# Kernel tuning notes

Measured on AMD Instinct MI355X. Metric: run time of the kernel, lower is better.

Reference implementation:

```python
import jax, jax.numpy as jnp
import numpy as np

E, D, H, K, N = 8, 512, 2048, 2, 1024  # experts, d_model, d_hidden, top_k, tokens
EPS = 1e-5


def _moe_linear(x, idx, W, b):
    # x: (M, in); idx: (M,) expert id per row; W: (E, out, in); b: (E, out)
    # Brute-force: compute per-expert dense GEMMs, select via one-hot (matches
    # BruteForceMoELinear math: y[i] = x[i] @ W[idx[i]].T + b[idx[i]]).
    m = jax.nn.one_hot(idx, W.shape[0], dtype=x.dtype)  # (M, E)
    y = jnp.einsum('me,eoi,mi->mo', m, W, x)
    return y + jnp.take(b, idx, axis=0)


def _forward(inp, gate_w, gate_b, w1, b1, w2, b2, ln_w, ln_b):
    # NaiveGate: linear -> top_k -> softmax over top-k logits
    logits = inp @ gate_w.T + gate_b              # (N, E)
    top_val, top_idx = jax.lax.top_k(logits, K)   # (N, K)
    score = jax.nn.softmax(top_val, axis=-1)      # (N, K)
    # repeat_interleave tokens, dispatch to experts
    x = jnp.repeat(inp, K, axis=0)                # (N*K, D)
    idx = top_idx.reshape(-1)                     # (N*K,)
    x = _moe_linear(x, idx, w1, b1)               # (N*K, H)
    x = jax.nn.gelu(x, approximate=False)         # torch F.gelu default = erf
    x = _moe_linear(x, idx, w2, b2)               # (N*K, D)
    x = x.reshape(N, K, D)
    x = jnp.einsum('nk,nkd->nd', score, x)        # bmm((N,1,K),(N,K,D)) combine
    # post layer norm (pre_lnorm=False)
    mu = jnp.mean(x, axis=-1, keepdims=True)
    var = jnp.var(x, axis=-1, keepdims=True)
    return (x - mu) * jax.lax.rsqrt(var + EPS) * ln_w + ln_b


def setup_inputs() -> dict:
    key = jax.random.key(0)
    ks = jax.random.split(key, 8)
    s = 0.02
    return {
        'inp': jax.random.normal(ks[0], (N, D), dtype=jnp.float32),
        'gate_w': s * jax.random.normal(ks[1], (E, D), dtype=jnp.float32),
        'gate_b': jnp.zeros((E,), dtype=jnp.float32),
        'w1': s * jax.random.normal(ks[2], (E, H, D), dtype=jnp.float32),
        'b1': jnp.zeros((E, H), dtype=jnp.float32),
        'w2': s * jax.random.normal(ks[3], (E, D, H), dtype=jnp.float32),
        'b2': jnp.zeros((E, D), dtype=jnp.float32),
        'ln_w': jnp.ones((D,), dtype=jnp.float32),
        'ln_b': jnp.zeros((D,), dtype=jnp.float32),
    }


def reference(inp, gate_w, gate_b, w1, b1, w2, b2, ln_w, ln_b):
    return _forward(inp, gate_w, gate_b, w1, b1, w2, b2, ln_w, ln_b)
```

## Files before the change

kernel.cpp:

```cpp
#include <hip/hip_runtime.h>
#include <cstdint>
#include <cstddef>

typedef _Float16 half_t;
typedef _Float16 half8 __attribute__((ext_vector_type(8)));
typedef float floatx4 __attribute__((ext_vector_type(4)));

#define E_ 8
#define D_ 512
#define H_ 2048
#define NTOK 1024
#define NP 2048
#define TM 128
#define MAX_TILES 24

__device__ __forceinline__ float gelu_f(float x) {
    return 0.5f * x * (1.0f + erff(x * 0.7071067811865476f));
}

__device__ __forceinline__ void gload_lds16(const half_t* g, half_t* l) {
    __builtin_amdgcn_global_load_lds(
        (__attribute__((address_space(1))) void*)(g),
        (__attribute__((address_space(3))) void*)(l),
        16, 0, 0);
}

__global__ __launch_bounds__(256) void gate_kernel(
        const float* __restrict__ inp, const float* __restrict__ gate_w,
        const float* __restrict__ gate_b, float* __restrict__ logits) {
    int n = blockIdx.x * 4 + (threadIdx.x >> 6);
    int lane = threadIdx.x & 63;
    const floatx4* xr = (const floatx4*)(inp + (size_t)n * D_);
    floatx4 x0 = xr[lane * 2], x1 = xr[lane * 2 + 1];
    #pragma unroll
    for (int e = 0; e < E_; e++) {
        const floatx4* gr = (const floatx4*)(gate_w + (size_t)e * D_);
        floatx4 g0 = gr[lane * 2], g1 = gr[lane * 2 + 1];
        float p = x0[0]*g0[0] + x0[1]*g0[1] + x0[2]*g0[2] + x0[3]*g0[3]
                + x1[0]*g1[0] + x1[1]*g1[1] + x1[2]*g1[2] + x1[3]*g1[3];
        #pragma unroll
        for (int m = 1; m < 64; m <<= 1) p += __shfl_xor(p, m);
        if (lane == 0) logits[(size_t)n * E_ + e] = p + gate_b[e];
    }
}

__global__ __launch_bounds__(256) void plan_kernel(
        const float* __restrict__ logits, float* __restrict__ score,
        int* __restrict__ idx, int* __restrict__ pos_of_pair,
        int* __restrict__ tile_e, int* __restrict__ tile_row0,
        int* __restrict__ tile_cnt, int* __restrict__ ntiles) {
    __shared__ int cnt_s[E_], off_s[E_ + 1], cur_s[E_];
    int tid = threadIdx.x;
    if (tid < E_) { cnt_s[tid] = 0; cur_s[tid] = 0; }
    __syncthreads();
    int my_e[4][2];
    #pragma unroll
    for (int i = 0; i < 4; i++) {
        int n = tid + i * 256;
        float l[E_];
        #pragma unroll
        for (int e = 0; e < E_; e++) l[e] = logits[(size_t)n * E_ + e];
        int e0 = 0; float v0 = l[0];
        #pragma unroll
        for (int e = 1; e < E_; e++) if (l[e] > v0) { v0 = l[e]; e0 = e; }
        int e1 = -1; float v1 = -3.4e38f;
        #pragma unroll
        for (int e = 0; e < E_; e++) if (e != e0 && l[e] > v1) { v1 = l[e]; e1 = e; }
        float s1 = expf(v1 - v0);
        float den = 1.0f + s1;
        score[2 * n]     = 1.0f / den;
        score[2 * n + 1] = s1 / den;
        idx[2 * n]     = e0;
        idx[2 * n + 1] = e1;
        atomicAdd(&cnt_s[e0], 1);
        atomicAdd(&cnt_s[e1], 1);
        my_e[i][0] = e0; my_e[i][1] = e1;
    }
    __syncthreads();
    if (tid == 0) {
        int o = 0;
        #pragma unroll
        for (int e = 0; e < E_; e++) { off_s[e] = o; o += cnt_s[e]; }
        off_s[E_] = o;
        int t = 0;
        for (int e = 0; e < E_; e++) {
            int c = cnt_s[e];
            int nt = (c + TM - 1) / TM;
            for (int i = 0; i < nt; i++) {
                tile_e[t] = e;
                tile_row0[t] = off_s[e] + i * TM;
                int rem = c - i * TM;
                tile_cnt[t] = rem < TM ? rem : TM;
                t++;
            }
        }
        ntiles[0] = t;
    }
    __syncthreads();
    #pragma unroll
    for (int i = 0; i < 4; i++) {
        #pragma unroll
        for (int k = 0; k < 2; k++) {
            int p = (tid + i * 256) * 2 + k;
            int e = my_e[i][k];
            int r = atomicAdd(&cur_s[e], 1);
            pos_of_pair[p] = off_s[e] + r;
        }
    }
}

__global__ __launch_bounds__(256) void scatter_kernel(
        const float* __restrict__ inp, const int* __restrict__ pos_of_pair,
        half_t* __restrict__ Xg) {
    int p = blockIdx.x * 4 + (threadIdx.x >> 6);
    int lane = threadIdx.x & 63;
    int pos = pos_of_pair[p];
    int n = p >> 1;
    const floatx4* src = (const floatx4*)(inp + (size_t)n * D_);
    floatx4 f0 = src[lane * 2], f1 = src[lane * 2 + 1];
    half8 h = { (half_t)f0[0], (half_t)f0[1], (half_t)f0[2], (half_t)f0[3],
                (half_t)f1[0], (half_t)f1[1], (half_t)f1[2], (half_t)f1[3] };
    *(half8*)(Xg + (size_t)pos * D_ + lane * 8) = h;
}

__global__ __launch_bounds__(256) void cvt_kernel(
        const float* __restrict__ w1, const float* __restrict__ w2,
        half_t* __restrict__ W1h, half_t* __restrict__ W2h) {
    const int n8 = E_ * H_ * D_ / 8;
    int i = blockIdx.x * 256 + threadIdx.x;
    const float* src; half_t* dst; int j;
    if (i < n8) { src = w1; dst = W1h; j = i; }
    else        { src = w2; dst = W2h; j = i - n8; }
    const floatx4* s = (const floatx4*)src + (size_t)j * 2;
    floatx4 f0 = s[0], f1 = s[1];
    half8 h = { (half_t)f0[0], (half_t)f0[1], (half_t)f0[2], (half_t)f0[3],
                (half_t)f1[0], (half_t)f1[1], (half_t)f1[2], (half_t)f1[3] };
    *(half8*)(dst + (size_t)j * 8) = h;
}

__global__ __launch_bounds__(256) void gemm1_kernel(
        const half_t* __restrict__ Xg, const half_t* __restrict__ W1h,
        const float* __restrict__ b1,
        const int* __restrict__ tile_e, const int* __restrict__ tile_row0,
        const int* __restrict__ tile_cnt, const int* __restrict__ ntiles,
        half_t* __restrict__ Y1) {
    __shared__ half_t As[TM * 32];
    __shared__ half_t Bs[128 * 32];
    int t = blockIdx.x;
    if (t >= ntiles[0]) return;
    int e = tile_e[t], row0 = tile_row0[t], cnt = tile_cnt[t];
    int colbase = blockIdx.y * 128;
    int tid = threadIdx.x;
    int wave = tid >> 6, lane = tid & 63;
    int quad = lane >> 4, l16 = lane & 15;
    int wm = (wave & 1) * 64, wn = (wave >> 1) * 64;

    int acol = (tid & 3) * 8;
    const half_t* Ag0 = Xg + (size_t)(row0 + (tid >> 2)) * D_ + acol;
    const half_t* Ag1 = Ag0 + 64 * D_;
    const half_t* Bg0 = W1h + ((size_t)e * H_ + colbase + (tid >> 2)) * D_ + acol;
    const half_t* Bg1 = Bg0 + 64 * D_;
    half_t* la0 = As + tid * 8;
    half_t* la1 = As + (tid + 256) * 8;
    half_t* lb0 = Bs + tid * 8;
    half_t* lb1 = Bs + (tid + 256) * 8;

    floatx4 acc[4][4] = {};
    for (int k0 = 0; k0 < D_; k0 += 32) {
        __syncthreads();
        gload_lds16(Ag0 + k0, la0);
        gload_lds16(Ag1 + k0, la1);
        gload_lds16(Bg0 + k0, lb0);
        gload_lds16(Bg1 + k0, lb1);
        __syncthreads();
        half8 a[4], b[4];
        #pragma unroll
        for (int mi = 0; mi < 4; mi++)
            a[mi] = *(const half8*)(As + (wm + mi * 16 + l16) * 32 + quad * 8);
        #pragma unroll
        for (int ni = 0; ni < 4; ni++)
            b[ni] = *(const half8*)(Bs + (wn + ni * 16 + l16) * 32 + quad * 8);
        #pragma unroll
        for (int mi = 0; mi < 4; mi++)
            #pragma unroll
            for (int ni = 0; ni < 4; ni++)
                acc[mi][ni] = __builtin_amdgcn_mfma_f32_16x16x32_f16(a[mi], b[ni], acc[mi][ni], 0, 0, 0);
    }
    float bias[4];
    #pragma unroll
    for (int ni = 0; ni < 4; ni++)
        bias[ni] = b1[(size_t)e * H_ + colbase + wn + ni * 16 + l16];
    #pragma unroll
    for (int mi = 0; mi < 4; mi++) {
        #pragma unroll
        for (int r = 0; r < 4; r++) {
            int rr = wm + mi * 16 + quad * 4 + r;
            if (rr >= cnt) continue;
            size_t rowoff = (size_t)(row0 + rr) * H_;
            #pragma unroll
            for (int ni = 0; ni < 4; ni++) {
                float v = acc[mi][ni][r] + bias[ni];
                Y1[rowoff + colbase + wn + ni * 16 + l16] = (half_t)gelu_f(v);
            }
        }
    }
}

__global__ __launch_bounds__(256) void gemm2_kernel(
        const half_t* __restrict__ Y1, const half_t* __restrict__ W2h,
        const int* __restrict__ tile_e, const int* __restrict__ tile_row0,
        const int* __restrict__ tile_cnt, const int* __restrict__ ntiles,
        float* __restrict__ Y2p) {
    __shared__ half_t As[TM * 32];
    __shared__ half_t Bs[128 * 32];
    int t = blockIdx.x;
    if (t >= ntiles[0]) return;
    int e = tile_e[t], row0 = tile_row0[t], cnt = tile_cnt[t];
    int colbase = blockIdx.y * 128;
    int kz = blockIdx.z;
    int kzbase = kz * 512;
    int tid = threadIdx.x;
    int wave = tid >> 6, lane = tid & 63;
    int quad = lane >> 4, l16 = lane & 15;
    int wm = (wave & 1) * 64, wn = (wave >> 1) * 64;

    int acol = (tid & 3) * 8;
    const half_t* Ag0 = Y1 + (size_t)(row0 + (tid >> 2)) * H_ + kzbase + acol;
    const half_t* Ag1 = Ag0 + 64 * H_;
    const half_t* Bg0 = W2h + ((size_t)e * D_ + colbase + (tid >> 2)) * H_ + kzbase + acol;
    const half_t* Bg1 = Bg0 + 64 * H_;
    half_t* la0 = As + tid * 8;
    half_t* la1 = As + (tid + 256) * 8;
    half_t* lb0 = Bs + tid * 8;
    half_t* lb1 = Bs + (tid + 256) * 8;

    floatx4 acc[4][4] = {};
    for (int k0 = 0; k0 < 512; k0 += 32) {
        __syncthreads();
        gload_lds16(Ag0 + k0, la0);
        gload_lds16(Ag1 + k0, la1);
        gload_lds16(Bg0 + k0, lb0);
        gload_lds16(Bg1 + k0, lb1);
        __syncthreads();
        half8 a[4], b[4];
        #pragma unroll
        for (int mi = 0; mi < 4; mi++)
            a[mi] = *(const half8*)(As + (wm + mi * 16 + l16) * 32 + quad * 8);
        #pragma unroll
        for (int ni = 0; ni < 4; ni++)
            b[ni] = *(const half8*)(Bs + (wn + ni * 16 + l16) * 32 + quad * 8);
        #pragma unroll
        for (int mi = 0; mi < 4; mi++)
            #pragma unroll
            for (int ni = 0; ni < 4; ni++)
                acc[mi][ni] = __builtin_amdgcn_mfma_f32_16x16x32_f16(a[mi], b[ni], acc[mi][ni], 0, 0, 0);
    }
    #pragma unroll
    for (int mi = 0; mi < 4; mi++) {
        #pragma unroll
        for (int r = 0; r < 4; r++) {
            int rr = wm + mi * 16 + quad * 4 + r;
            if (rr >= cnt) continue;
            size_t rowoff = ((size_t)kz * NP + row0 + rr) * D_;
            #pragma unroll
            for (int ni = 0; ni < 4; ni++)
                Y2p[rowoff + colbase + wn + ni * 16 + l16] = acc[mi][ni][r];
        }
    }
}

__global__ __launch_bounds__(256) void final_kernel(
        const float* __restrict__ Y2p, const float* __restrict__ b2,
        const int* __restrict__ idx, const float* __restrict__ score,
        const int* __restrict__ pos_of_pair,
        const float* __restrict__ ln_w, const float* __restrict__ ln_b,
        float* __restrict__ out) {
    int n = blockIdx.x * 4 + (threadIdx.x >> 6);
    int lane = threadIdx.x & 63;
    int p0 = pos_of_pair[2 * n], p1 = pos_of_pair[2 * n + 1];
    int e0 = idx[2 * n], e1 = idx[2 * n + 1];
    float s0 = score[2 * n], s1 = score[2 * n + 1];

    const floatx4* b2r0 = (const floatx4*)(b2 + (size_t)e0 * D_);
    const floatx4* b2r1 = (const floatx4*)(b2 + (size_t)e1 * D_);
    floatx4 a_lo = b2r0[lane * 2], a_hi = b2r0[lane * 2 + 1];
    floatx4 c_lo = b2r1[lane * 2], c_hi = b2r1[lane * 2 + 1];
    #pragma unroll
    for (int kz = 0; kz < 4; kz++) {
        const floatx4* r0 = (const floatx4*)(Y2p + ((size_t)kz * NP + p0) * D_);
        const floatx4* r1 = (const floatx4*)(Y2p + ((size_t)kz * NP + p1) * D_);
        a_lo += r0[lane * 2]; a_hi += r0[lane * 2 + 1];
        c_lo += r1[lane * 2]; c_hi += r1[lane * 2 + 1];
    }
    floatx4 y_lo = s0 * a_lo + s1 * c_lo;
    floatx4 y_hi = s0 * a_hi + s1 * c_hi;

    float s = 0.0f, q = 0.0f;
    #pragma unroll
    for (int j = 0; j < 4; j++) {
        s += y_lo[j] + y_hi[j];
        q += y_lo[j] * y_lo[j] + y_hi[j] * y_hi[j];
    }
    #pragma unroll
    for (int m = 1; m < 64; m <<= 1) {
        s += __shfl_xor(s, m);
        q += __shfl_xor(q, m);
    }
    float mean = s * (1.0f / 512.0f);
    float var = q * (1.0f / 512.0f) - mean * mean;
    float inv = 1.0f / sqrtf(var + 1e-5f);

    const floatx4* wv = (const floatx4*)ln_w;
    const floatx4* bv = (const floatx4*)ln_b;
    floatx4 o_lo = (y_lo - mean) * inv * wv[lane * 2]     + bv[lane * 2];
    floatx4 o_hi = (y_hi - mean) * inv * wv[lane * 2 + 1] + bv[lane * 2 + 1];
    floatx4* op = (floatx4*)(out + (size_t)n * D_);
    op[lane * 2] = o_lo;
    op[lane * 2 + 1] = o_hi;
}

extern "C" void kernel_launch(void* const* d_in, const int* in_sizes, int n_in,
                              void* d_out, int out_size, void* d_ws, size_t ws_size,
                              hipStream_t stream) {
    const float* inp    = (const float*)d_in[0];
    const float* gate_w = (const float*)d_in[1];
    const float* gate_b = (const float*)d_in[2];
    const float* w1     = (const float*)d_in[3];
    const float* b1     = (const float*)d_in[4];
    const float* w2     = (const float*)d_in[5];
    const float* b2     = (const float*)d_in[6];
    const float* ln_w   = (const float*)d_in[7];
    const float* ln_b   = (const float*)d_in[8];
    float* out = (float*)d_out;

    char* ws = (char*)d_ws;
    size_t o = 0;
    auto carve = [&](size_t bytes) -> char* {
        char* p = ws + o;
        o += (bytes + 255) & ~(size_t)255;
        return p;
    };
    half_t* W1h = (half_t*)carve(sizeof(half_t) * (size_t)E_ * H_ * D_);
    half_t* W2h = (half_t*)carve(sizeof(half_t) * (size_t)E_ * D_ * H_);
    half_t* Xg  = (half_t*)carve(sizeof(half_t) * (size_t)(NP + TM) * D_);
    half_t* Y1  = (half_t*)carve(sizeof(half_t) * (size_t)(NP + TM) * H_);
    float*  Y2p = (float*)carve(sizeof(float) * 4 * (size_t)NP * D_);
    float*  logits = (float*)carve(sizeof(float) * NTOK * E_);
    float*  score  = (float*)carve(sizeof(float) * NP);
    int* idx         = (int*)carve(sizeof(int) * NP);
    int* pos_of_pair = (int*)carve(sizeof(int) * NP);
    int* tile_e      = (int*)carve(sizeof(int) * MAX_TILES);
    int* tile_row0   = (int*)carve(sizeof(int) * MAX_TILES);
    int* tile_cnt    = (int*)carve(sizeof(int) * MAX_TILES);
    int* ntiles      = (int*)carve(sizeof(int) * 1);

    gate_kernel<<<NTOK / 4, 256, 0, stream>>>(inp, gate_w, gate_b, logits);
    plan_kernel<<<1, 256, 0, stream>>>(logits, score, idx, pos_of_pair,
                                       tile_e, tile_row0, tile_cnt, ntiles);
    scatter_kernel<<<NP / 4, 256, 0, stream>>>(inp, pos_of_pair, Xg);
    cvt_kernel<<<2 * E_ * H_ * D_ / 8 / 256, 256, 0, stream>>>(w1, w2, W1h, W2h);
    gemm1_kernel<<<dim3(MAX_TILES, H_ / 128), 256, 0, stream>>>(
        Xg, W1h, b1, tile_e, tile_row0, tile_cnt, ntiles, Y1);
    gemm2_kernel<<<dim3(MAX_TILES, D_ / 128, 4), 256, 0, stream>>>(
        Y1, W2h, tile_e, tile_row0, tile_cnt, ntiles, Y2p);
    final_kernel<<<NTOK / 4, 256, 0, stream>>>(Y2p, b2, idx, score, pos_of_pair, ln_w, ln_b, out);
}
```

Measured before the change: 170.1 us.

## Fuse gating, routing and scatter; use fixed per-expert capacity slots in GEMMs

After: 206.6 us. 21.4% more time.

```diff
diff --git a/kernel.cpp b/kernel.cpp
--- a/kernel.cpp
+++ b/kernel.cpp
@@ -11,8 +11,8 @@
 #define H_ 2048
 #define NTOK 1024
 #define NP 2048
+#define CAP 1024
 #define TM 128
-#define MAX_TILES 24
 
 __device__ __forceinline__ float gelu_f(float x) {
     return 0.5f * x * (1.0f + erff(x * 0.7071067811865476f));
@@ -25,13 +25,34 @@
         16, 0, 0);
 }
 
-__global__ __launch_bounds__(256) void gate_kernel(
+__global__ __launch_bounds__(256) void cvt_kernel(
+        const float* __restrict__ w1, const float* __restrict__ w2,
+        half_t* __restrict__ W1h, half_t* __restrict__ W2h,
+        int* __restrict__ cnt_g) {
+    if (blockIdx.x == 0 && threadIdx.x < E_) cnt_g[threadIdx.x] = 0;
+    const int NG = E_ * H_ * D_ / 8;
+    int i = blockIdx.x * 256 + threadIdx.x;
+    const float* src; half_t* dst; int j;
+    if (i < NG) { src = w1; dst = W1h; j = i; }
+    else        { src = w2; dst = W2h; j = i - NG; }
+    const floatx4* s = (const floatx4*)src + (size_t)j * 2;
+    floatx4 f0 = s[0], f1 = s[1];
+    half8 h = { (half_t)f0[0], (half_t)f0[1], (half_t)f0[2], (half_t)f0[3],
+                (half_t)f1[0], (half_t)f1[1], (half_t)f1[2], (half_t)f1[3] };
+    *(half8*)(dst + (size_t)j * 8) = h;
+}
+
+__global__ __launch_bounds__(256) void gate_scatter_kernel(
         const float* __restrict__ inp, const float* __restrict__ gate_w,
-        const float* __restrict__ gate_b, float* __restrict__ logits) {
+        const float* __restrict__ gate_b,
+        float* __restrict__ score, int* __restrict__ idx,
+        int* __restrict__ pos_of_pair, int* __restrict__ cnt_g,
+        half_t* __restrict__ Xg) {
     int n = blockIdx.x * 4 + (threadIdx.x >> 6);
     int lane = threadIdx.x & 63;
     const floatx4* xr = (const floatx4*)(inp + (size_t)n * D_);
     floatx4 x0 = xr[lane * 2], x1 = xr[lane * 2 + 1];
+    float l[E_];
     #pragma unroll
     for (int e = 0; e < E_; e++) {
         const floatx4* gr = (const floatx4*)(gate_w + (size_t)e * D_);
@@ -40,151 +61,85 @@
                 + x1[0]*g1[0] + x1[1]*g1[1] + x1[2]*g1[2] + x1[3]*g1[3];
         #pragma unroll
         for (int m = 1; m < 64; m <<= 1) p += __shfl_xor(p, m);
-        if (lane == 0) logits[(size_t)n * E_ + e] = p + gate_b[e];
-    }
-}
-
-__global__ __launch_bounds__(256) void plan_kernel(
-        const float* __restrict__ logits, float* __restrict__ score,
-        int* __restrict__ idx, int* __restrict__ pos_of_pair,
-        int* __restrict__ tile_e, int* __restrict__ tile_row0,
-        int* __restrict__ tile_cnt, int* __restrict__ ntiles) {
-    __shared__ int cnt_s[E_], off_s[E_ + 1], cur_s[E_];
-    int tid = threadIdx.x;
-    if (tid < E_) { cnt_s[tid] = 0; cur_s[tid] = 0; }
-    __syncthreads();
-    int my_e[4][2];
-    #pragma unroll
-    for (int i = 0; i < 4; i++) {
-        int n = tid + i * 256;
-        float l[E_];
-        #pragma unroll
-        for (int e = 0; e < E_; e++) l[e] = logits[(size_t)n * E_ + e];
-        int e0 = 0; float v0 = l[0];
-        #pragma unroll
-        for (int e = 1; e < E_; e++) if (l[e] > v0) { v0 = l[e]; e0 = e; }
-        int e1 = -1; float v1 = -3.4e38f;
-        #pragma unroll
-        for (int e = 0; e < E_; e++) if (e != e0 && l[e] > v1) { v1 = l[e]; e1 = e; }
+        l[e] = p + gate_b[e];
+    }
+    int e0 = 0; float v0 = l[0];
+    #pragma unroll
+    for (int e = 1; e < E_; e++) if (l[e] > v0) { v0 = l[e]; e0 = e; }
+    int e1 = -1; float v1 = -3.4e38f;
+    #pragma unroll
+    for (int e = 0; e < E_; e++) if (e != e0 && l[e] > v1) { v1 = l[e]; e1 = e; }
+    int p0 = 0, p1 = 0;
+    if (lane == 0) {
         float s1 = expf(v1 - v0);
         float den = 1.0f + s1;
         score[2 * n]     = 1.0f / den;
         score[2 * n + 1] = s1 / den;
         idx[2 * n]     = e0;
         idx[2 * n + 1] = e1;
-        atomicAdd(&cnt_s[e0], 1);
-        atomicAdd(&cnt_s[e1], 1);
-        my_e[i][0] = e0; my_e[i][1] = e1;
-    }
-    __syncthreads();
-    if (tid == 0) {
-        int o = 0;
-        #pragma unroll
-        for (int e = 0; e < E_; e++) { off_s[e] = o; o += cnt_s[e]; }
-        off_s[E_] = o;
-        int t = 0;
-        for (int e = 0; e < E_; e++) {
-            int c = cnt_s[e];
-            int nt = (c + TM - 1) / TM;
-            for (int i = 0; i < nt; i++) {
-                tile_e[t] = e;
-                tile_row0[t] = off_s[e] + i * TM;
-                int rem = c - i * TM;
-                tile_cnt[t] = rem < TM ? rem : TM;
-                t++;
-            }
-        }
-        ntiles[0] = t;
-    }
-    __syncthreads();
-    #pragma unroll
-    for (int i = 0; i < 4; i++) {
-        #pragma unroll
-        for (int k = 0; k < 2; k++) {
-            int p = (tid + i * 256) * 2 + k;
-            int e = my_e[i][k];
-            int r = atomicAdd(&cur_s[e], 1);
-            pos_of_pair[p] = off_s[e] + r;
-        }
-    }
-}
-
-__global__ __launch_bounds__(256) void scatter_kernel(
-        const float* __restrict__ inp, const int* __restrict__ pos_of_pair,
-        half_t* __restrict__ Xg) {
-    int p = blockIdx.x * 4 + (threadIdx.x >> 6);
-    int lane = threadIdx.x & 63;
-    int pos = pos_of_pair[p];
-    int n = p >> 1;
-    const floatx4* src = (const floatx4*)(inp + (size_t)n * D_);
-    floatx4 f0 = src[lane * 2], f1 = src[lane * 2 + 1];
-    half8 h = { (half_t)f0[0], (half_t)f0[1], (half_t)f0[2], (half_t)f0[3],
-                (half_t)f1[0], (half_t)f1[1], (half_t)f1[2], (half_t)f1[3] };
-    *(half8*)(Xg + (size_t)pos * D_ + lane * 8) = h;
-}
-
-__global__ __launch_bounds__(256) void cvt_kernel(
-        const float* __restrict__ w1, const float* __restrict__ w2,
-        half_t* __restrict__ W1h, half_t* __restrict__ W2h) {
-    const int n8 = E_ * H_ * D_ / 8;
-    int i = blockIdx.x * 256 + threadIdx.x;
-    const float* src; half_t* dst; int j;
-    if (i < n8) { src = w1; dst = W1h; j = i; }
-    else        { src = w2; dst = W2h; j = i - n8; }
-    const floatx4* s = (const floatx4*)src + (size_t)j * 2;
-    floatx4 f0 = s[0], f1 = s[1];
-    half8 h = { (half_t)f0[0], (half_t)f0[1], (half_t)f0[2], (half_t)f0[3],
-                (half_t)f1[0], (half_t)f1[1], (half_t)f1[2], (half_t)f1[3] };
-    *(half8*)(dst + (size_t)j * 8) = h;
-}
-
-__global__ __launch_bounds__(256) void gemm1_kernel(
+        p0 = e0 * CAP + atomicAdd(&cnt_g[e0], 1);
+        p1 = e1 * CAP + atomicAdd(&cnt_g[e1], 1);
+        pos_of_pair[2 * n]     = p0;
+        pos_of_pair[2 * n + 1] = p1;
+    }
+    p0 = __shfl(p0, 0);
+    p1 = __shfl(p1, 0);
+    half8 h = { (half_t)x0[0], (half_t)x0[1], (half_t)x0[2], (half_t)x0[3],
+                (half_t)x1[0], (half_t)x1[1], (half_t)x1[2], (half_t)x1[3] };
+    *(half8*)(Xg + (size_t)p0 * D_ + lane * 8) = h;
+    *(half8*)(Xg + (size_t)p1 * D_ + lane * 8) = h;
+}
+
+__global__ __launch_bounds__(256, 2) void gemm1_kernel(
         const half_t* __restrict__ Xg, const half_t* __restrict__ W1h,
-        const float* __restrict__ b1,
-        const int* __restrict__ tile_e, const int* __restrict__ tile_row0,
-        const int* __restrict__ tile_cnt, const int* __restrict__ ntiles,
+        const float* __restrict__ b1, const int* __restrict__ cnt_g,
         half_t* __restrict__ Y1) {
-    __shared__ half_t As[TM * 32];
-    __shared__ half_t Bs[128 * 32];
-    int t = blockIdx.x;
-    if (t >= ntiles[0]) return;
-    int e = tile_e[t], row0 = tile_row0[t], cnt = tile_cnt[t];
+    __shared__ half_t As[2 * 128 * 32];
+    __shared__ half_t Bs[2 * 128 * 32];
+    int slot = blockIdx.x;
+    int e = slot >> 3, ti = slot & 7;
+    int valid = cnt_g[e] - ti * TM;
+    if (valid <= 0) return;
+    int cnt = valid < TM ? valid : TM;
+    int row0 = e * CAP + ti * TM;
     int colbase = blockIdx.y * 128;
     int tid = threadIdx.x;
-    int wave = tid >> 6, lane = tid & 63;
-    int quad = lane >> 4, l16 = lane & 15;
+    int wave = tid >> 6, lane = tid & 63, quad = lane >> 4, l16 = lane & 15;
     int wm = (wave & 1) * 64, wn = (wave >> 1) * 64;
-
-    int acol = (tid & 3) * 8;
-    const half_t* Ag0 = Xg + (size_t)(row0 + (tid >> 2)) * D_ + acol;
-    const half_t* Ag1 = Ag0 + 64 * D_;
-    const half_t* Bg0 = W1h + ((size_t)e * H_ + colbase + (tid >> 2)) * D_ + acol;
-    const half_t* Bg1 = Bg0 + 64 * D_;
-    half_t* la0 = As + tid * 8;
-    half_t* la1 = As + (tid + 256) * 8;
-    half_t* lb0 = Bs + tid * 8;
-    half_t* lb1 = Bs + (tid + 256) * 8;
-
+    const half_t* Abase = Xg + (size_t)row0 * D_;
+    const half_t* Bbase = W1h + ((size_t)e * H_ + colbase) * D_;
+    int srow = tid >> 2, scol = (tid & 3) * 8;
     floatx4 acc[4][4] = {};
-    for (int k0 = 0; k0 < D_; k0 += 32) {
+    for (int k0 = 0; k0 < D_; k0 += 64) {
         __syncthreads();
-        gload_lds16(Ag0 + k0, la0);
-        gload_lds16(Ag1 + k0, la1);
-        gload_lds16(Bg0 + k0, lb0);
-        gload_lds16(Bg1 + k0, lb1);
+        #pragma unroll
+        for (int j = 0; j < 2; j++) {
+            #pragma unroll
+            for (int s = 0; s < 2; s++) {
+                int q = tid + s * 256;
+                int row = srow + s * 64;
+                gload_lds16(Abase + (size_t)row * D_ + k0 + j * 32 + scol,
+                            As + j * 4096 + q * 8);
+                gload_lds16(Bbase + (size_t)row * D_ + k0 + j * 32 + scol,
+                            Bs + j * 4096 + q * 8);
+            }
+        }
         __syncthreads();
-        half8 a[4], b[4];
-        #pragma unroll
-        for (int mi = 0; mi < 4; mi++)
-            a[mi] = *(const half8*)(As + (wm + mi * 16 + l16) * 32 + quad * 8);
-        #pragma unroll
-        for (int ni = 0; ni < 4; ni++)
-            b[ni] = *(const half8*)(Bs + (wn + ni * 16 + l16) * 32 + quad * 8);
-        #pragma unroll
-        for (int mi = 0; mi < 4; mi++)
+        #pragma unroll
+        for (int j = 0; j < 2; j++) {
+            half8 a[4], b[4];
+            #pragma unroll
+            for (int mi = 0; mi < 4; mi++)
+                a[mi] = *(const half8*)(As + j * 4096 + (wm + mi * 16 + l16) * 32 + quad * 8);
             #pragma unroll
             for (int ni = 0; ni < 4; ni++)
-                acc[mi][ni] = __builtin_amdgcn_mfma_f32_16x16x32_f16(a[mi], b[ni], acc[mi][ni], 0, 0, 0);
+                b[ni] = *(const half8*)(Bs + j * 4096 + (wn + ni * 16 + l16) * 32 + quad * 8);
+            #pragma unroll
+            for (int mi = 0; mi < 4; mi++)
+                #pragma unroll
+                for (int ni = 0; ni < 4; ni++)
+                    acc[mi][ni] = __builtin_amdgcn_mfma_f32_16x16x32_f16(a[mi], b[ni], acc[mi][ni], 0, 0, 0);
+        }
     }
     float bias[4];
     #pragma unroll
@@ -206,54 +161,57 @@
     }
 }
 
-__global__ __launch_bounds__(256) void gemm2_kernel(
+__global__ __launch_bounds__(256, 2) void gemm2_kernel(
         const half_t* __restrict__ Y1, const half_t* __restrict__ W2h,
-        const int* __restrict__ tile_e, const int* __restrict__ tile_row0,
-        const int* __restrict__ tile_cnt, const int* __restrict__ ntiles,
-        float* __restrict__ Y2p) {
-    __shared__ half_t As[TM * 32];
-    __shared__ half_t Bs[128 * 32];
-    int t = blockIdx.x;
-    if (t >= ntiles[0]) return;
-    int e = tile_e[t], row0 = tile_row0[t], cnt = tile_cnt[t];
+        const int* __restrict__ cnt_g, float* __restrict__ Y2p) {
+    __shared__ half_t As[2 * 128 * 32];
+    __shared__ half_t Bs[2 * 128 * 32];
+    int slot = blockIdx.x;
+    int e = slot >> 3, ti = slot & 7;
+    int valid = cnt_g[e] - ti * TM;
+    if (valid <= 0) return;
+    int cnt = valid < TM ? valid : TM;
+    int row0 = e * CAP + ti * TM;
     int colbase = blockIdx.y * 128;
     int kz = blockIdx.z;
-    int kzbase = kz * 512;
+    int kzb = kz * 512;
     int tid = threadIdx.x;
-    int wave = tid >> 6, lane = tid & 63;
-    int quad = lane >> 4, l16 = lane & 15;
+    int wave = tid >> 6, lane = tid & 63, quad = lane >> 4, l16 = lane & 15;
     int wm = (wave & 1) * 64, wn = (wave >> 1) * 64;
-
-    int acol = (tid & 3) * 8;
-    const half_t* Ag0 = Y1 + (size_t)(row0 + (tid >> 2)) * H_ + kzbase + acol;
-    const half_t* Ag1 = Ag0 + 64 * H_;
-    const half_t* Bg0 = W2h + ((size_t)e * D_ + colbase + (tid >> 2)) * H_ + kzbase + acol;
-    const half_t* Bg1 = Bg0 + 64 * H_;
-    half_t* la0 = As + tid * 8;
-    half_t* la1 = As + (tid + 256) * 8;
-    half_t* lb0 = Bs + tid * 8;
-    half_t* lb1 = Bs + (tid + 256) * 8;
-
+    const half_t* Abase = Y1 + (size_t)row0 * H_ + kzb;
+    const half_t* Bbase = W2h + ((size_t)e * D_ + colbase) * H_ + kzb;
+    int srow = tid >> 2, scol = (tid & 3) * 8;
     floatx4 acc[4][4] = {};
-    for (int k0 = 0; k0 < 512; k0 += 32) {
+    for (int k0 = 0; k0 < 512; k0 += 64) {
         __syncthreads();
-        gload_lds16(Ag0 + k0, la0);
-        gload_lds16(Ag1 + k0, la1);
-        gload_lds16(Bg0 + k0, lb0);
-        gload_lds16(Bg1 + k0, lb1);
+        #pragma unroll
+        for (int j = 0; j < 2; j++) {
+            #pragma unroll
+            for (int s = 0; s < 2; s++) {
+                int q = tid + s * 256;
+                int row = srow + s * 64;
+                gload_lds16(Abase + (size_t)row * H_ + k0 + j * 32 + scol,
+                            As + j * 4096 + q * 8);
+                gload_lds16(Bbase + (size_t)row * H_ + k0 + j * 32 + scol,
+                            Bs + j * 4096 + q * 8);
+            }
+        }
         __syncthreads();
-        half8 a[4], b[4];
-        #pragma unroll
-        for (int mi = 0; mi < 4; mi++)
-            a[mi] = *(const half8*)(As + (wm + mi * 16 + l16) * 32 + quad * 8);
-        #pragma unroll
-        for (int ni = 0; ni < 4; ni++)
-            b[ni] = *(const half8*)(Bs + (wn + ni * 16 + l16) * 32 + quad * 8);
-        #pragma unroll
-        for (int mi = 0; mi < 4; mi++)
+        #pragma unroll
+        for (int j = 0; j < 2; j++) {
+            half8 a[4], b[4];
+            #pragma unroll
+            for (int mi = 0; mi < 4; mi++)
+                a[mi] = *(const half8*)(As + j * 4096 + (wm + mi * 16 + l16) * 32 + quad * 8);
             #pragma unroll
             for (int ni = 0; ni < 4; ni++)
-                acc[mi][ni] = __builtin_amdgcn_mfma_f32_16x16x32_f16(a[mi], b[ni], acc[mi][ni], 0, 0, 0);
+                b[ni] = *(const half8*)(Bs + j * 4096 + (wn + ni * 16 + l16) * 32 + quad * 8);
+            #pragma unroll
+            for (int mi = 0; mi < 4; mi++)
+                #pragma unroll
+                for (int ni = 0; ni < 4; ni++)
+                    acc[mi][ni] = __builtin_amdgcn_mfma_f32_16x16x32_f16(a[mi], b[ni], acc[mi][ni], 0, 0, 0);
+        }
     }
     #pragma unroll
     for (int mi = 0; mi < 4; mi++) {
@@ -261,7 +219,7 @@
         for (int r = 0; r < 4; r++) {
             int rr = wm + mi * 16 + quad * 4 + r;
             if (rr >= cnt) continue;
-            size_t rowoff = ((size_t)kz * NP + row0 + rr) * D_;
+            size_t rowoff = ((size_t)kz * (E_ * CAP) + row0 + rr) * D_;
             #pragma unroll
             for (int ni = 0; ni < 4; ni++)
                 Y2p[rowoff + colbase + wn + ni * 16 + l16] = acc[mi][ni][r];
@@ -287,8 +245,8 @@
     floatx4 c_lo = b2r1[lane * 2], c_hi = b2r1[lane * 2 + 1];
     #pragma unroll
     for (int kz = 0; kz < 4; kz++) {
-        const floatx4* r0 = (const floatx4*)(Y2p + ((size_t)kz * NP + p0) * D_);
-        const floatx4* r1 = (const floatx4*)(Y2p + ((size_t)kz * NP + p1) * D_);
+        const floatx4* r0 = (const floatx4*)(Y2p + ((size_t)kz * (E_ * CAP) + p0) * D_);
+        const floatx4* r1 = (const floatx4*)(Y2p + ((size_t)kz * (E_ * CAP) + p1) * D_);
         a_lo += r0[lane * 2]; a_hi += r0[lane * 2 + 1];
         c_lo += r1[lane * 2]; c_hi += r1[lane * 2 + 1];
     }
@@ -342,26 +300,20 @@
     };
     half_t* W1h = (half_t*)carve(sizeof(half_t) * (size_t)E_ * H_ * D_);
     half_t* W2h = (half_t*)carve(sizeof(half_t) * (size_t)E_ * D_ * H_);
-    half_t* Xg  = (half_t*)carve(sizeof(half_t) * (size_t)(NP + TM) * D_);
-    half_t* Y1  = (half_t*)carve(sizeof(half_t) * (size_t)(NP + TM) * H_);
-    float*  Y2p = (float*)carve(sizeof(float) * 4 * (size_t)NP * D_);
-    float*  logits = (float*)carve(sizeof(float) * NTOK * E_);
-    float*  score  = (float*)carve(sizeof(float) * NP);
+    half_t* Xg  = (half_t*)carve(sizeof(half_t) * (size_t)E_ * CAP * D_);
+    half_t* Y1  = (half_t*)carve(sizeof(half_t) * (size_t)E_ * CAP * H_);
+    float*  Y2p = (float*)carve(sizeof(float) * 4 * (size_t)E_ * CAP * D_);
+    float*  score = (float*)carve(sizeof(float) * NP);
     int* idx         = (int*)carve(sizeof(int) * NP);
     int* pos_of_pair = (int*)carve(sizeof(int) * NP);
-    int* tile_e      = (int*)carve(sizeof(int) * MAX_TILES);
-    int* tile_row0   = (int*)carve(sizeof(int) * MAX_TILES);
-    int* tile_cnt    = (int*)carve(sizeof(int) * MAX_TILES);
-    int* ntiles      = (int*)carve(sizeof(int) * 1);
-
-    gate_kernel<<<NTOK / 4, 256, 0, stream>>>(inp, gate_w, gate_b, logits);
-    plan_kernel<<<1, 256, 0, stream>>>(logits, score, idx, pos_of_pair,
-                                       tile_e, tile_row0, tile_cnt, ntiles);
-    scatter_kernel<<<NP / 4, 256, 0, stream>>>(inp, pos_of_pair, Xg);
-    cvt_kernel<<<2 * E_ * H_ * D_ / 8 / 256, 256, 0, stream>>>(w1, w2, W1h, W2h);
-    gemm1_kernel<<<dim3(MAX_TILES, H_ / 128), 256, 0, stream>>>(
-        Xg, W1h, b1, tile_e, tile_row0, tile_cnt, ntiles, Y1);
-    gemm2_kernel<<<dim3(MAX_TILES, D_ / 128, 4), 256, 0, stream>>>(
-        Y1, W2h, tile_e, tile_row0, tile_cnt, ntiles, Y2p);
+    int* cnt_g       = (int*)carve(sizeof(int) * E_);
+
+    cvt_kernel<<<2 * E_ * H_ * D_ / 8 / 256, 256, 0, stream>>>(w1, w2, W1h, W2h, cnt_g);
+    gate_scatter_kernel<<<NTOK / 4, 256, 0, stream>>>(inp, gate_w, gate_b,
+                                                      score, idx, pos_of_pair, cnt_g, Xg);
+    gemm1_kernel<<<dim3(E_ * (CAP / TM), H_ / 128), 256, 0, stream>>>(
+        Xg, W1h, b1, cnt_g, Y1);
+    gemm2_kernel<<<dim3(E_ * (CAP / TM), D_ / 128, 4), 256, 0, stream>>>(
+        Y1, W2h, cnt_g, Y2p);
     final_kernel<<<NTOK / 4, 256, 0, stream>>>(Y2p, b2, idx, score, pos_of_pair, ln_w, ln_b, out);
 }
```
